# Performance work log

Hardware: AMD Instinct MI355X
Metric: run time of the kernel (lower is better)

## Reference

```python
import jax, jax.numpy as jnp
import numpy as np

NU, NI, D, C, V, E, L = 100000, 50000, 128, 5, 200000, 200000, 10


def setup_inputs() -> dict:
    key = jax.random.key(0)
    ks = jax.random.split(key, 16)
    s = lambda fan_in: 1.0 / np.sqrt(fan_in)
    return {
        "urf": jax.random.normal(ks[0], (NU, D), jnp.float32),
        "irf": jax.random.normal(ks[1], (NI, D), jnp.float32),
        "utf": jax.random.normal(ks[2], (NU, D), jnp.float32),
        "itf": jax.random.normal(ks[3], (NI, D), jnp.float32),
        "w1r": jax.random.normal(ks[4], (2 * D, D), jnp.float32) * s(2 * D),
        "w2r": jax.random.normal(ks[5], (D, D), jnp.float32) * s(D),
        "w1t": jax.random.normal(ks[6], (2 * D, D), jnp.float32) * s(2 * D),
        "w2t": jax.random.normal(ks[7], (D, D), jnp.float32) * s(D),
        "wp": jax.random.normal(ks[8], (D, C), jnp.float32) * s(D),
        "emb": jax.random.normal(ks[9], (V, D), jnp.float32),
        "src": jax.random.randint(ks[10], (E,), 0, NU, jnp.int32),
        "dst": jax.random.randint(ks[11], (E,), 0, NI, jnp.int32),
        "sentence_id": jax.random.randint(ks[12], (E, L), 0, V, jnp.int32),
        "neg_sid": jax.random.randint(ks[13], (E, L), 1, V, jnp.int32),
    }


def _review_feature(emb, sid):
    # masked mean-pool of sentence embeddings: [E, L] -> [E, D]
    length = (sid > 0).astype(jnp.float32).sum(axis=-1, keepdims=True) + 1e-9
    return emb[sid].sum(axis=-2) / length


def reference(urf, irf, utf, itf, w1r, w2r, w1t, w2t, wp, emb,
              src, dst, sentence_id, neg_sid):
    # edge-wise gather of src (user) / dst (item) features + concat  [E, 2D]
    rf = jnp.concatenate([urf[src], irf[dst]], axis=1)
    rh = jax.nn.relu(rf @ w1r) @ w2r                      # rating_linear  [E, D]
    pr = rh @ wp                                          # rating_predictor [E, C]
    tf = jnp.concatenate([utf[src], itf[dst]], axis=1)
    th = jax.nn.relu(tf @ w1t) @ w2t + rh                 # topic_linear + residual
    pos_review = _review_feature(emb, sentence_id)        # [E, D]
    neg_review = _review_feature(emb, neg_sid)            # [E, D]
    pos_score = (th * pos_review).sum(axis=1)             # [E]
    neg_score = (th * neg_review).sum(axis=1)
    loss = -jax.nn.log_sigmoid(pos_score - neg_score)     # -log(sigmoid(pos-neg))
    return pr, loss.mean(), loss.mean()
```

## Files before the change

kernel.cpp:

```cpp
#include <hip/hip_runtime.h>

#define NU_ 100000
#define NI_ 50000
#define D_  128
#define C_  5
#define V_  200000
#define E_  200000
#define L_  10

typedef __bf16 bf16x8 __attribute__((ext_vector_type(8)));
typedef unsigned short u16;
typedef u16 u16x8 __attribute__((ext_vector_type(8)));
typedef float f32x4 __attribute__((ext_vector_type(4)));

#define W1R_OFF 0
#define W2R_OFF 32768
#define W1T_OFF 49152
#define W2T_OFF 81920
#define WTOT    98304

__device__ __forceinline__ u16 f2bf(float x) {
    union { float f; unsigned int u; } v; v.f = x;
    unsigned int u = v.u;
    return (u16)((u + 0x7FFFu + ((u >> 16) & 1u)) >> 16);
}

__global__ void prep_kernel(const float* __restrict__ w1r, const float* __restrict__ w2r,
                            const float* __restrict__ w1t, const float* __restrict__ w2t,
                            u16* __restrict__ wbuf, float* __restrict__ loss_acc) {
    int idx = blockIdx.x * blockDim.x + threadIdx.x;
    if (idx == 0) *loss_acc = 0.f;
    if (idx >= WTOT) return;
    const float* src; int base;
    if (idx < W2R_OFF)      { src = w1r; base = W1R_OFF; }
    else if (idx < W1T_OFF) { src = w2r; base = W2R_OFF; }
    else if (idx < W2T_OFF) { src = w1t; base = W1T_OFF; }
    else                    { src = w2t; base = W2T_OFF; }
    int local = idx - base;
    int j = local & 7;
    int g = local >> 3;
    int n = g & 127;
    int kq = g >> 7;
    int k = kq * 8 + j;
    wbuf[idx] = f2bf(src[k * 128 + n]);
}

__device__ __forceinline__ void stage_pair(const float* __restrict__ ut,
                                           const float* __restrict__ it,
                                           const int* __restrict__ srcI,
                                           const int* __restrict__ dstI,
                                           int ebase, int lane, u16* buf) {
    int m = lane >> 2;
    int part = lane & 3;
    int e = ebase + m;
    const float* row = (part < 2) ? (ut + (size_t)srcI[e] * D_)
                                  : (it + (size_t)dstI[e] * D_);
    const float* seg = row + (part & 1) * 64;
    int k8base = part * 8;
#pragma unroll
    for (int i = 0; i < 8; i++) {
        float4 a = *(const float4*)(seg + i * 8);
        float4 b = *(const float4*)(seg + i * 8 + 4);
        u16x8 v;
        v[0] = f2bf(a.x); v[1] = f2bf(a.y); v[2] = f2bf(a.z); v[3] = f2bf(a.w);
        v[4] = f2bf(b.x); v[5] = f2bf(b.y); v[6] = f2bf(b.z); v[7] = f2bf(b.w);
        *(u16x8*)(buf + ((k8base + i) * 16 + m) * 8) = v;
    }
}

template <int KT>
__device__ __forceinline__ void gemm_tile(const u16* aLDS, const u16* __restrict__ Wg,
                                          int lq, int ln, f32x4 acc[8]) {
#pragma unroll
    for (int kt = 0; kt < KT; kt++) {
        bf16x8 af = *(const bf16x8*)(aLDS + ((kt * 4 + lq) * 16 + ln) * 8);
#pragma unroll
        for (int nt = 0; nt < 8; nt++) {
            bf16x8 bfv = *(const bf16x8*)(Wg + (size_t)((kt * 4 + lq) * 128 + nt * 16 + ln) * 8);
            acc[nt] = __builtin_amdgcn_mfma_f32_16x16x32_bf16(af, bfv, acc[nt], 0, 0, 0);
        }
    }
}

__device__ __forceinline__ void store_h_relu(const f32x4 acc[8], u16* buf, int lq, int ln) {
#pragma unroll
    for (int nt = 0; nt < 8; nt++) {
#pragma unroll
        for (int reg = 0; reg < 4; reg++) {
            float h = fmaxf(acc[nt][reg], 0.f);
            int dcol = nt * 16 + ln;
            int r = lq * 4 + reg;
            buf[((dcol >> 3) * 16 + r) * 8 + (dcol & 7)] = f2bf(h);
        }
    }
}

__global__ __launch_bounds__(256, 3) void fused_kernel(
    const float* __restrict__ urf, const float* __restrict__ irf,
    const float* __restrict__ utf, const float* __restrict__ itf,
    const float* __restrict__ wp, const float* __restrict__ emb,
    const int* __restrict__ srcI, const int* __restrict__ dstI,
    const int* __restrict__ sidI, const int* __restrict__ nsidI,
    const u16* __restrict__ wbuf, float* __restrict__ loss_acc,
    float* __restrict__ out) {
    __shared__ u16 smem[4 * 6144];
    const int tid = threadIdx.x;
    const int w = tid >> 6;
    const int lane = tid & 63;
    const int lq = lane >> 4;
    const int ln = lane & 15;
    u16* bufA = smem + w * 6144;
    u16* bufB = bufA + 4096;
    const int ebase = blockIdx.x * 64 + w * 16;

    stage_pair(urf, irf, srcI, dstI, ebase, lane, bufA);
    __syncthreads();

    f32x4 rh[8];
    {
        f32x4 acc[8];
#pragma unroll
        for (int nt = 0; nt < 8; nt++) acc[nt] = (f32x4){0.f, 0.f, 0.f, 0.f};
        gemm_tile<8>(bufA, wbuf + W1R_OFF, lq, ln, acc);
        store_h_relu(acc, bufB, lq, ln);
    }
    __syncthreads();
    {
#pragma unroll
        for (int nt = 0; nt < 8; nt++) rh[nt] = (f32x4){0.f, 0.f, 0.f, 0.f};
        gemm_tile<4>(bufB, wbuf + W2R_OFF, lq, ln, rh);
    }

    {
        float pp[4][5];
#pragma unroll
        for (int r = 0; r < 4; r++)
#pragma unroll
            for (int c = 0; c < 5; c++) pp[r][c] = 0.f;
#pragma unroll
        for (int nt = 0; nt < 8; nt++) {
            int d = nt * 16 + ln;
            float wpc[5];
#pragma unroll
            for (int c = 0; c < 5; c++) wpc[c] = wp[d * 5 + c];
#pragma unroll
            for (int reg = 0; reg < 4; reg++)
#pragma unroll
                for (int c = 0; c < 5; c++) pp[reg][c] += rh[nt][reg] * wpc[c];
        }
#pragma unroll
        for (int off = 1; off < 16; off <<= 1)
#pragma unroll
            for (int reg = 0; reg < 4; reg++)
#pragma unroll
                for (int c = 0; c < 5; c++)
                    pp[reg][c] += __shfl_xor(pp[reg][c], off, 64);
        if (ln == 0) {
#pragma unroll
            for (int reg = 0; reg < 4; reg++) {
                int e = ebase + lq * 4 + reg;
#pragma unroll
                for (int c = 0; c < 5; c++) out[(size_t)e * 5 + c] = pp[reg][c];
            }
        }
    }

    __syncthreads();
    stage_pair(utf, itf, srcI, dstI, ebase, lane, bufA);
    __syncthreads();
    f32x4 acc[8];
    {
#pragma unroll
        for (int nt = 0; nt < 8; nt++) acc[nt] = (f32x4){0.f, 0.f, 0.f, 0.f};
        gemm_tile<8>(bufA, wbuf + W1T_OFF, lq, ln, acc);
        store_h_relu(acc, bufB, lq, ln);
    }
    __syncthreads();
#pragma unroll
    for (int nt = 0; nt < 8; nt++) acc[nt] = rh[nt];
    gemm_tile<4>(bufB, wbuf + W2T_OFF, lq, ln, acc);

    float* thb = (float*)bufA;
#pragma unroll
    for (int nt = 0; nt < 8; nt++)
#pragma unroll
        for (int reg = 0; reg < 4; reg++)
            thb[(lq * 4 + reg) * 128 + nt * 16 + ln] = acc[nt][reg];
    __syncthreads();

    float wave_loss = 0.f;
    for (int m = 0; m < 16; m++) {
        int e = ebase + m;
        float2 t = *(const float2*)(thb + m * 128 + lane * 2);
        float p0 = 0.f, p1 = 0.f, q0 = 0.f, q1 = 0.f;
        int pcnt = 0, ncnt = 0;
#pragma unroll
        for (int i = 0; i < L_; i++) {
            int s = sidI[e * L_ + i];
            pcnt += (s > 0) ? 1 : 0;
            float2 ev = *(const float2*)(emb + (size_t)s * D_ + lane * 2);
            p0 += ev.x; p1 += ev.y;
        }
#pragma unroll
        for (int i = 0; i < L_; i++) {
            int s = nsidI[e * L_ + i];
            ncnt += (s > 0) ? 1 : 0;
            float2 ev = *(const float2*)(emb + (size_t)s * D_ + lane * 2);
            q0 += ev.x; q1 += ev.y;
        }
        float ps = t.x * p0 + t.y * p1;
        float ns = t.x * q0 + t.y * q1;
#pragma unroll
        for (int off = 1; off < 64; off <<= 1) {
            ps += __shfl_xor(ps, off, 64);
            ns += __shfl_xor(ns, off, 64);
        }
        ps /= ((float)pcnt + 1e-9f);
        ns /= ((float)ncnt + 1e-9f);
        float x = ns - ps;
        wave_loss += fmaxf(x, 0.f) + log1pf(expf(-fabsf(x)));
    }
    if (lane == 0) atomicAdd(loss_acc, wave_loss);
}

__global__ void finish_kernel(const float* __restrict__ loss_acc, float* __restrict__ out) {
    float v = loss_acc[0] * (1.0f / (float)E_);
    out[(size_t)E_ * C_]     = v;
    out[(size_t)E_ * C_ + 1] = v;
}

extern "C" void kernel_launch(void* const* d_in, const int* in_sizes, int n_in,
                              void* d_out, int out_size, void* d_ws, size_t ws_size,
                              hipStream_t stream) {
    const float* urf = (const float*)d_in[0];
    const float* irf = (const float*)d_in[1];
    const float* utf = (const float*)d_in[2];
    const float* itf = (const float*)d_in[3];
    const float* w1r = (const float*)d_in[4];
    const float* w2r = (const float*)d_in[5];
    const float* w1t = (const float*)d_in[6];
    const float* w2t = (const float*)d_in[7];
    const float* wp  = (const float*)d_in[8];
    const float* emb = (const float*)d_in[9];
    const int* srcI  = (const int*)d_in[10];
    const int* dstI  = (const int*)d_in[11];
    const int* sidI  = (const int*)d_in[12];
    const int* nsidI = (const int*)d_in[13];
    float* out = (float*)d_out;

    float* loss_acc = (float*)d_ws;
    u16* wbuf = (u16*)((char*)d_ws + 256);

    prep_kernel<<<(WTOT + 255) / 256, 256, 0, stream>>>(w1r, w2r, w1t, w2t, wbuf, loss_acc);
    fused_kernel<<<E_ / 64, 256, 0, stream>>>(urf, irf, utf, itf, wp, emb,
                                              srcI, dstI, sidI, nsidI,
                                              wbuf, loss_acc, out);
    finish_kernel<<<1, 1, 0, stream>>>(loss_acc, out);
}
```

Baseline: 631.5 us.

## Split first-layer GEMM into two K halves to shrink LDS and raise occupancy

```diff
diff --git a/kernel.cpp b/kernel.cpp
--- a/kernel.cpp
+++ b/kernel.cpp
@@ -41,30 +41,20 @@
     int g = local >> 3;
     int n = g & 127;
     int kq = g >> 7;
-    int k = kq * 8 + j;
-    wbuf[idx] = f2bf(src[k * 128 + n]);
-}
-
-__device__ __forceinline__ void stage_pair(const float* __restrict__ ut,
-                                           const float* __restrict__ it,
-                                           const int* __restrict__ srcI,
-                                           const int* __restrict__ dstI,
-                                           int ebase, int lane, u16* buf) {
-    int m = lane >> 2;
-    int part = lane & 3;
-    int e = ebase + m;
-    const float* row = (part < 2) ? (ut + (size_t)srcI[e] * D_)
-                                  : (it + (size_t)dstI[e] * D_);
-    const float* seg = row + (part & 1) * 64;
-    int k8base = part * 8;
-#pragma unroll
-    for (int i = 0; i < 8; i++) {
+    wbuf[idx] = f2bf(src[(kq * 8 + j) * 128 + n]);
+}
+
+__device__ __forceinline__ void stage_half(const float* __restrict__ row, int lane, u16* buf) {
+    int m = lane >> 2, q = lane & 3;
+    const float* seg = row + q * 32;
+#pragma unroll
+    for (int i = 0; i < 4; i++) {
         float4 a = *(const float4*)(seg + i * 8);
         float4 b = *(const float4*)(seg + i * 8 + 4);
         u16x8 v;
         v[0] = f2bf(a.x); v[1] = f2bf(a.y); v[2] = f2bf(a.z); v[3] = f2bf(a.w);
         v[4] = f2bf(b.x); v[5] = f2bf(b.y); v[6] = f2bf(b.z); v[7] = f2bf(b.w);
-        *(u16x8*)(buf + ((k8base + i) * 16 + m) * 8) = v;
+        *(u16x8*)(buf + ((q * 4 + i) * 16 + m) * 8) = v;
     }
 }
 
@@ -84,7 +74,7 @@
 
 __device__ __forceinline__ void store_h_relu(const f32x4 acc[8], u16* buf, int lq, int ln) {
 #pragma unroll
-    for (int nt = 0; nt < 8; nt++) {
+    for (int nt = 0; nt < 8; nt++)
 #pragma unroll
         for (int reg = 0; reg < 4; reg++) {
             float h = fmaxf(acc[nt][reg], 0.f);
@@ -92,10 +82,36 @@
             int r = lq * 4 + reg;
             buf[((dcol >> 3) * 16 + r) * 8 + (dcol & 7)] = f2bf(h);
         }
-    }
-}
-
-__global__ __launch_bounds__(256, 3) void fused_kernel(
+}
+
+__device__ __forceinline__ void mlp(const float* __restrict__ uF, const float* __restrict__ iF,
+                                    const int* __restrict__ srcI, const int* __restrict__ dstI,
+                                    int ebase, int lane, int lq, int ln,
+                                    const u16* __restrict__ w1, const u16* __restrict__ w2,
+                                    u16* bufA, u16* bufB, f32x4 acc[8]) {
+    int e = ebase + (lane >> 2);
+    int su = srcI[e], sd = dstI[e];
+    f32x4 h1[8];
+#pragma unroll
+    for (int nt = 0; nt < 8; nt++) h1[nt] = (f32x4){0.f, 0.f, 0.f, 0.f};
+
+    stage_half(uF + (size_t)su * D_, lane, bufA);
+    __syncthreads();
+    gemm_tile<4>(bufA, w1, lq, ln, h1);
+    __syncthreads();
+    stage_half(iF + (size_t)sd * D_, lane, bufA);
+    __syncthreads();
+    gemm_tile<4>(bufA, w1 + 16384, lq, ln, h1);
+    store_h_relu(h1, bufB, lq, ln);
+    __syncthreads();
+    gemm_tile<4>(bufB, w2, lq, ln, acc);
+}
+
+__device__ __forceinline__ float softplus_(float x) {
+    return fmaxf(x, 0.f) + log1pf(expf(-fabsf(x)));
+}
+
+__global__ __launch_bounds__(256, 5) void fused_kernel(
     const float* __restrict__ urf, const float* __restrict__ irf,
     const float* __restrict__ utf, const float* __restrict__ itf,
     const float* __restrict__ wp, const float* __restrict__ emb,
@@ -103,33 +119,21 @@
     const int* __restrict__ sidI, const int* __restrict__ nsidI,
     const u16* __restrict__ wbuf, float* __restrict__ loss_acc,
     float* __restrict__ out) {
-    __shared__ u16 smem[4 * 6144];
+    __shared__ u16 smem[4 * 4096];
     const int tid = threadIdx.x;
     const int w = tid >> 6;
     const int lane = tid & 63;
     const int lq = lane >> 4;
     const int ln = lane & 15;
-    u16* bufA = smem + w * 6144;
-    u16* bufB = bufA + 4096;
+    u16* bufA = smem + w * 4096;
+    u16* bufB = bufA + 2048;
     const int ebase = blockIdx.x * 64 + w * 16;
 
-    stage_pair(urf, irf, srcI, dstI, ebase, lane, bufA);
-    __syncthreads();
-
     f32x4 rh[8];
-    {
-        f32x4 acc[8];
-#pragma unroll
-        for (int nt = 0; nt < 8; nt++) acc[nt] = (f32x4){0.f, 0.f, 0.f, 0.f};
-        gemm_tile<8>(bufA, wbuf + W1R_OFF, lq, ln, acc);
-        store_h_relu(acc, bufB, lq, ln);
-    }
-    __syncthreads();
-    {
-#pragma unroll
-        for (int nt = 0; nt < 8; nt++) rh[nt] = (f32x4){0.f, 0.f, 0.f, 0.f};
-        gemm_tile<4>(bufB, wbuf + W2R_OFF, lq, ln, rh);
-    }
+#pragma unroll
+    for (int nt = 0; nt < 8; nt++) rh[nt] = (f32x4){0.f, 0.f, 0.f, 0.f};
+    mlp(urf, irf, srcI, dstI, ebase, lane, lq, ln,
+        wbuf + W1R_OFF, wbuf + W2R_OFF, bufA, bufB, rh);
 
     {
         float pp[4][5];
@@ -166,60 +170,57 @@
     }
 
     __syncthreads();
-    stage_pair(utf, itf, srcI, dstI, ebase, lane, bufA);
-    __syncthreads();
-    f32x4 acc[8];
-    {
-#pragma unroll
-        for (int nt = 0; nt < 8; nt++) acc[nt] = (f32x4){0.f, 0.f, 0.f, 0.f};
-        gemm_tile<8>(bufA, wbuf + W1T_OFF, lq, ln, acc);
-        store_h_relu(acc, bufB, lq, ln);
-    }
-    __syncthreads();
-#pragma unroll
-    for (int nt = 0; nt < 8; nt++) acc[nt] = rh[nt];
-    gemm_tile<4>(bufB, wbuf + W2T_OFF, lq, ln, acc);
-
+    f32x4 th[8];
+#pragma unroll
+    for (int nt = 0; nt < 8; nt++) th[nt] = rh[nt];
+    mlp(utf, itf, srcI, dstI, ebase, lane, lq, ln,
+        wbuf + W1T_OFF, wbuf + W2T_OFF, bufA, bufB, th);
+
+    __syncthreads();
     float* thb = (float*)bufA;
 #pragma unroll
     for (int nt = 0; nt < 8; nt++)
 #pragma unroll
         for (int reg = 0; reg < 4; reg++)
-            thb[(lq * 4 + reg) * 128 + nt * 16 + ln] = acc[nt][reg];
+            thb[(lq * 4 + reg) * 128 + nt * 16 + ln] = th[nt][reg];
     __syncthreads();
 
     float wave_loss = 0.f;
-    for (int m = 0; m < 16; m++) {
+    const int h = lane >> 5, hl = lane & 31;
+    for (int mp = 0; mp < 16; mp += 2) {
+        int m = mp + h;
         int e = ebase + m;
-        float2 t = *(const float2*)(thb + m * 128 + lane * 2);
-        float p0 = 0.f, p1 = 0.f, q0 = 0.f, q1 = 0.f;
+        float4 t4 = *(const float4*)(thb + m * 128 + hl * 4);
+        const int* sp = sidI + e * L_;
+        const int* np = nsidI + e * L_;
+        float ps = 0.f, ns = 0.f;
         int pcnt = 0, ncnt = 0;
 #pragma unroll
         for (int i = 0; i < L_; i++) {
-            int s = sidI[e * L_ + i];
+            int s = sp[i];
             pcnt += (s > 0) ? 1 : 0;
-            float2 ev = *(const float2*)(emb + (size_t)s * D_ + lane * 2);
-            p0 += ev.x; p1 += ev.y;
+            float4 ev = *(const float4*)(emb + (size_t)s * D_ + hl * 4);
+            ps += t4.x * ev.x + t4.y * ev.y + t4.z * ev.z + t4.w * ev.w;
         }
 #pragma unroll
         for (int i = 0; i < L_; i++) {
-            int s = nsidI[e * L_ + i];
+            int s = np[i];
             ncnt += (s > 0) ? 1 : 0;
-            float2 ev = *(const float2*)(emb + (size_t)s * D_ + lane * 2);
-            q0 += ev.x; q1 += ev.y;
-        }
-        float ps = t.x * p0 + t.y * p1;
-        float ns = t.x * q0 + t.y * q1;
-#pragma unroll
-        for (int off = 1; off < 64; off <<= 1) {
+            float4 ev = *(const float4*)(emb + (size_t)s * D_ + hl * 4);
+            ns += t4.x * ev.x + t4.y * ev.y + t4.z * ev.z + t4.w * ev.w;
+        }
+#pragma unroll
+        for (int off = 1; off < 32; off <<= 1) {
             ps += __shfl_xor(ps, off, 64);
             ns += __shfl_xor(ns, off, 64);
         }
-        ps /= ((float)pcnt + 1e-9f);
-        ns /= ((float)ncnt + 1e-9f);
-        float x = ns - ps;
-        wave_loss += fmaxf(x, 0.f) + log1pf(expf(-fabsf(x)));
-    }
+        if (hl == 0) {
+            ps /= ((float)pcnt + 1e-9f);
+            ns /= ((float)ncnt + 1e-9f);
+            wave_loss += softplus_(ns - ps);
+        }
+    }
+    wave_loss += __shfl_xor(wave_loss, 32, 64);
     if (lane == 0) atomicAdd(loss_acc, wave_loss);
 }
 
```

Measured after the change: 765.4 us. +21.2%, slower.
